# Kernel tuning notes

Hardware: AMD Instinct MI355X
Metric: run time of the kernel (lower is better)

The kernel has to match this reference:

```python
import jax, jax.numpy as jnp
import numpy as np

INITIAL_CAPITAL = 500.0
TRANSACTION_COST = 0.0003
TAU = 1.0  # gumbel-softmax temperature
B, S, F = 256, 4096, 64


def setup_inputs() -> dict:
    key = jax.random.key(0)
    ks = jax.random.split(key, 10)
    features = jax.random.normal(ks[0], (B, S, F), dtype=jnp.float32)
    # make columns 1/2 look like vix level / vix change so branches fire
    features = features.at[:, :, 1].set(20.0 + 10.0 * jax.random.uniform(ks[1], (B, S)))
    features = features.at[:, :, 2].set(0.5 * jax.random.normal(ks[2], (B, S)))
    features = features.at[:, :, 3].set(0.01 * jax.random.normal(ks[3], (B, S)))
    return {
        "features": features,
        "feature_weights": jnp.ones((F,), jnp.float32) / F,
        "long_threshold": jnp.float32(0.52),
        "short_threshold": jnp.float32(0.48),
        "base_position_size": jnp.float32(0.8),
        "conviction_scalar": jnp.float32(0.5),
        "vix_impact": jnp.float32(0.2),
        "vix_collapse_threshold": jnp.float32(0.15),
        "vix_spike_threshold": jnp.float32(0.15),
        "gumbel_noise": jax.random.gumbel(ks[4], (S, B, 3), dtype=jnp.float32),
    }


def reference(features, feature_weights, long_threshold, short_threshold,
              base_position_size, conviction_scalar, vix_impact,
              vix_collapse_threshold, vix_spike_threshold, gumbel_noise):
    batch, seq_len, _ = features.shape
    # predictions: sigmoid of feature-weighted sum  [B,S]
    predictions = jax.nn.sigmoid(jnp.einsum('bsf,f->bs', features, feature_weights))
    # time-major per-step inputs [S,B]
    pred_t = predictions.T
    mom_t = features[:, :, 0].T
    vix_t = features[:, :, 1].T
    vch_t = features[:, :, 2].T
    mret_t = features[:, :, 3].T

    def step(carry, x):
        eq, pos = carry  # eq [B], pos [B,3]
        p, v, dv, m, r, g = x
        signal_strength = jnp.abs(p - 0.5) / 0.5
        vix_collapse = (dv < -vix_collapse_threshold) & (v < 30.0)
        vix_spike = (dv > vix_spike_threshold) & (v > 20.0)
        psz = jnp.clip(base_position_size + conviction_scalar * signal_strength, 0.2, 1.0)
        psz = jnp.where(vix_collapse | vix_spike, psz * (1.0 + vix_impact), psz)
        long_pos = ((p >= long_threshold) & (m > 0)) | vix_collapse
        short_pos = ((p <= short_threshold) & (m < 0)) | vix_spike
        logits = jnp.stack([
            jnp.where(long_pos, 1.0, -10.0),
            jnp.where(short_pos, 1.0, -10.0),
            jnp.where(~long_pos & ~short_pos, 1.0, -10.0),
        ], axis=1)  # [B,3]
        probs = jax.nn.softmax((logits + g) / TAU, axis=1)
        strategy_return = psz * (probs[:, 0] - probs[:, 1]) * r
        position_change = jnp.abs(probs - pos).sum(axis=1)
        eq_new = eq * (1.0 + strategy_return - position_change * TRANSACTION_COST)
        return (eq_new, probs), (eq_new, probs, psz)

    eq0 = jnp.full((batch,), INITIAL_CAPITAL, dtype=features.dtype)
    pos0 = jnp.zeros((batch, 3), features.dtype).at[:, 2].set(1.0)
    (_, _), (eq_seq, pos_seq, psz_seq) = jax.lax.scan(
        step, (eq0, pos0), (pred_t, vix_t, vch_t, mom_t, mret_t, gumbel_noise))
    equity = jnp.concatenate([eq0[:, None], eq_seq.T], axis=1)          # [B,S+1]
    positions = jnp.concatenate([pos0[:, None], jnp.swapaxes(pos_seq, 0, 1)], axis=1)  # [B,S+1,3]
    position_sizes = psz_seq[-1]  # last timestep, matching torch loop leak
    return equity, positions, predictions, position_sizes
```

## Files before the change

### kernel.cpp

```cpp
#include <hip/hip_runtime.h>

#define Bn 256
#define Sn 4096
#define Fn 64
#define TCOST 0.0003f
#define INIT_CAP 500.0f

#define EQ_OFF   0
#define POS_OFF  (Bn * (Sn + 1))
#define PRED_OFF (Bn * (Sn + 1) * 4)
#define PSZ_OFF  (PRED_OFF + Bn * Sn)

#define ROWS_PB 64

__global__ __launch_bounds__(256) void trishot_fwd(
    const float* __restrict__ feat,
    const float* __restrict__ w,
    const float* __restrict__ p_lt, const float* __restrict__ p_st,
    const float* __restrict__ p_bps, const float* __restrict__ p_cs,
    const float* __restrict__ p_vi, const float* __restrict__ p_vct,
    const float* __restrict__ p_vst,
    const float* __restrict__ gumbel,
    float* __restrict__ out)
{
    const int tid  = threadIdx.x;
    const int lane = tid & 63;
    const int wave = tid >> 6;
    const int sub  = lane & 15;
    const int grp  = lane >> 4;

    const float LT = *p_lt, ST = *p_st, BPS = *p_bps, CS = *p_cs,
                VI = *p_vi, VCT = *p_vct, VST = *p_vst;

    const float4 wv = ((const float4*)w)[sub];

    const size_t r0 = (size_t)blockIdx.x * ROWS_PB;

#pragma unroll
    for (int pass = 0; pass < ROWS_PB / 16; ++pass) {
        const size_t row = r0 + (size_t)pass * 16 + (size_t)(wave * 4 + grp);
        const float4 fv = ((const float4*)feat)[row * 16 + sub];

        float x = fv.x * wv.x + fv.y * wv.y + fv.z * wv.z + fv.w * wv.w;
        x += __shfl_xor(x, 1);
        x += __shfl_xor(x, 2);
        x += __shfl_xor(x, 4);
        x += __shfl_xor(x, 8);

        if (sub == 0) {
            const int b = (int)(row >> 12);
            const int s = (int)(row & (Sn - 1));

            const float p = 1.0f / (1.0f + __expf(-x));
            const float mom = fv.x, vix = fv.y, dvix = fv.z, mret = fv.w;

            const float ss = fabsf(p - 0.5f) * 2.0f;
            const bool collapse = (dvix < -VCT) && (vix < 30.0f);
            const bool spike    = (dvix >  VST) && (vix > 20.0f);
            float psz = fminf(fmaxf(BPS + CS * ss, 0.2f), 1.0f);
            if (collapse || spike) psz *= (1.0f + VI);

            const bool lp = ((p >= LT) && (mom > 0.0f)) || collapse;
            const bool sp = ((p <= ST) && (mom < 0.0f)) || spike;
            const float l0 = lp ? 1.0f : -10.0f;
            const float l1 = sp ? 1.0f : -10.0f;
            const float l2 = (!lp && !sp) ? 1.0f : -10.0f;

            const float* g = gumbel + ((size_t)s * Bn + b) * 3;
            const float z0 = l0 + g[0], z1 = l1 + g[1], z2 = l2 + g[2];
            const float zm = fmaxf(z0, fmaxf(z1, z2));
            const float e0 = __expf(z0 - zm), e1 = __expf(z1 - zm),
                        e2 = __expf(z2 - zm);
            const float inv = 1.0f / (e0 + e1 + e2);
            const float q0 = e0 * inv, q1 = e1 * inv, q2 = e2 * inv;

            out[PRED_OFF + row] = p;

            const size_t prow = ((size_t)b * (Sn + 1) + s + 1) * 3;
            float* pos = out + POS_OFF;
            pos[prow + 0] = q0;
            pos[prow + 1] = q1;
            pos[prow + 2] = q2;

            out[EQ_OFF + (size_t)b * (Sn + 1) + s + 1] = psz * (q0 - q1) * mret;

            if (s == 0) {
                const size_t p0row = (size_t)b * (Sn + 1) * 3;
                pos[p0row + 0] = 0.0f;
                pos[p0row + 1] = 0.0f;
                pos[p0row + 2] = 1.0f;
            }
            if (s == Sn - 1) {
                out[PSZ_OFF + b] = psz;
            }
        }
    }
}

#define TB   1024
#define CHB  (Sn / TB)
#define PADi(i) ((i) + ((i) >> 3))

__global__ __launch_bounds__(TB) void trishot_scan(float* __restrict__ out)
{
    const int b = blockIdx.x;
    const int j = threadIdx.x;
    const int lane = j & 63;
    const int wid  = j >> 6;

    float* eq = out + EQ_OFF + (size_t)b * (Sn + 1);
    const float* pos = out + POS_OFF + (size_t)b * (Sn + 1) * 3;

    __shared__ float sfac[Sn + (Sn >> 3)];
    __shared__ float swave[16];

    for (int i = j; i < Sn; i += TB) {
        const float a0 = pos[i * 3 + 0];
        const float a1 = pos[i * 3 + 1];
        const float a2 = pos[i * 3 + 2];
        const float c0 = pos[i * 3 + 3];
        const float c1 = pos[i * 3 + 4];
        const float c2 = pos[i * 3 + 5];
        const float pc = fabsf(c0 - a0) + fabsf(c1 - a1) + fabsf(c2 - a2);
        const float rp = eq[i + 1];
        sfac[PADi(i)] = 1.0f + rp - pc * TCOST;
    }
    __syncthreads();

    const int t0 = j * CHB;
    const float f0 = sfac[PADi(t0 + 0)];
    const float f1 = sfac[PADi(t0 + 1)];
    const float f2 = sfac[PADi(t0 + 2)];
    const float f3 = sfac[PADi(t0 + 3)];
    const float lprod = f0 * f1 * f2 * f3;

    float incl = lprod;
#pragma unroll
    for (int off = 1; off < 64; off <<= 1) {
        const float v = __shfl_up(incl, off);
        if (lane >= off) incl *= v;
    }
    if (lane == 63) swave[wid] = incl;
    __syncthreads();

    if (wid == 0) {
        float wv = (lane < 16) ? swave[lane] : 1.0f;
#pragma unroll
        for (int off = 1; off < 16; off <<= 1) {
            const float v = __shfl_up(wv, off);
            if (lane >= off) wv *= v;
        }
        if (lane < 16) swave[lane] = wv;
    }
    __syncthreads();

    const float woff = (wid > 0) ? swave[wid - 1] : 1.0f;
    float excl = __shfl_up(incl, 1);
    if (lane == 0) excl = 1.0f;
    float eqv = INIT_CAP * woff * excl;
    eqv *= f0; eq[t0 + 1] = eqv;
    eqv *= f1; eq[t0 + 2] = eqv;
    eqv *= f2; eq[t0 + 3] = eqv;
    eqv *= f3; eq[t0 + 4] = eqv;
    if (j == 0) eq[0] = INIT_CAP;
}

extern "C" void kernel_launch(void* const* d_in, const int* in_sizes, int n_in,
                              void* d_out, int out_size, void* d_ws, size_t ws_size,
                              hipStream_t stream) {
    const float* feat   = (const float*)d_in[0];
    const float* w      = (const float*)d_in[1];
    const float* lt     = (const float*)d_in[2];
    const float* st     = (const float*)d_in[3];
    const float* bps    = (const float*)d_in[4];
    const float* cs     = (const float*)d_in[5];
    const float* vi     = (const float*)d_in[6];
    const float* vct    = (const float*)d_in[7];
    const float* vst    = (const float*)d_in[8];
    const float* gumbel = (const float*)d_in[9];
    float* out = (float*)d_out;

    trishot_fwd<<<(Bn * Sn) / ROWS_PB, 256, 0, stream>>>(
        feat, w, lt, st, bps, cs, vi, vct, vst, gumbel, out);
    trishot_scan<<<Bn, TB, 0, stream>>>(out);
}
```

Baseline: 388.1 us.

## Compute per-step equity factors in forward kernel to skip scan's positions reread

The forward kernel now keeps each block's softmax probabilities and raw returns in shared memory and writes the full per-step multiplicative factor, including the transaction cost term. It recomputes the previous row's probabilities for the block boundary. The scan kernel then reads the factors directly instead of rereading the positions array (3 floats per step) and building a shared-memory factor buffer. This removes a large global read in the scan and its LDS staging, at the cost of a small redundant computation and an extra barrier per forward block.

Measured after the change: 386.9 us. About the same (-0.3%).

```diff
diff --git a/kernel.cpp b/kernel.cpp
--- a/kernel.cpp
+++ b/kernel.cpp
@@ -29,16 +29,56 @@
     const int sub  = lane & 15;
     const int grp  = lane >> 4;
 
+    __shared__ float sq0[ROWS_PB + 1];
+    __shared__ float sq1[ROWS_PB + 1];
+    __shared__ float sq2[ROWS_PB + 1];
+    __shared__ float srp[ROWS_PB];
+
     const float LT = *p_lt, ST = *p_st, BPS = *p_bps, CS = *p_cs,
                 VI = *p_vi, VCT = *p_vct, VST = *p_vst;
 
     const float4 wv = ((const float4*)w)[sub];
 
     const size_t r0 = (size_t)blockIdx.x * ROWS_PB;
+    const int b  = (int)(r0 >> 12);
+    const int s0 = (int)(r0 & (Sn - 1));
+
+    if (tid < 16) {
+        float q0p = 0.0f, q1p = 0.0f, q2p = 1.0f;
+        if (s0 != 0) {
+            const float4 fvp = ((const float4*)feat)[(r0 - 1) * 16 + sub];
+            float xp = fvp.x * wv.x + fvp.y * wv.y + fvp.z * wv.z
+                     + fvp.w * wv.w;
+            xp += __shfl_xor(xp, 1);
+            xp += __shfl_xor(xp, 2);
+            xp += __shfl_xor(xp, 4);
+            xp += __shfl_xor(xp, 8);
+            if (tid == 0) {
+                const float p = 1.0f / (1.0f + __expf(-xp));
+                const float mom = fvp.x, vix = fvp.y, dvix = fvp.z;
+                const bool collapse = (dvix < -VCT) && (vix < 30.0f);
+                const bool spike    = (dvix >  VST) && (vix > 20.0f);
+                const bool lp = ((p >= LT) && (mom > 0.0f)) || collapse;
+                const bool sp = ((p <= ST) && (mom < 0.0f)) || spike;
+                const float l0 = lp ? 1.0f : -10.0f;
+                const float l1 = sp ? 1.0f : -10.0f;
+                const float l2 = (!lp && !sp) ? 1.0f : -10.0f;
+                const float* g = gumbel + ((size_t)(s0 - 1) * Bn + b) * 3;
+                const float z0 = l0 + g[0], z1 = l1 + g[1], z2 = l2 + g[2];
+                const float zm = fmaxf(z0, fmaxf(z1, z2));
+                const float e0 = __expf(z0 - zm), e1 = __expf(z1 - zm),
+                            e2 = __expf(z2 - zm);
+                const float inv = 1.0f / (e0 + e1 + e2);
+                q0p = e0 * inv; q1p = e1 * inv; q2p = e2 * inv;
+            }
+        }
+        if (tid == 0) { sq0[0] = q0p; sq1[0] = q1p; sq2[0] = q2p; }
+    }
 
 #pragma unroll
     for (int pass = 0; pass < ROWS_PB / 16; ++pass) {
-        const size_t row = r0 + (size_t)pass * 16 + (size_t)(wave * 4 + grp);
+        const int ridx = pass * 16 + wave * 4 + grp;
+        const size_t row = r0 + (size_t)ridx;
         const float4 fv = ((const float4*)feat)[row * 16 + sub];
 
         float x = fv.x * wv.x + fv.y * wv.y + fv.z * wv.z + fv.w * wv.w;
@@ -48,8 +88,7 @@
         x += __shfl_xor(x, 8);
 
         if (sub == 0) {
-            const int b = (int)(row >> 12);
-            const int s = (int)(row & (Sn - 1));
+            const int s = s0 + ridx;
 
             const float p = 1.0f / (1.0f + __expf(-x));
             const float mom = fv.x, vix = fv.y, dvix = fv.z, mret = fv.w;
@@ -82,24 +121,29 @@
             pos[prow + 1] = q1;
             pos[prow + 2] = q2;
 
-            out[EQ_OFF + (size_t)b * (Sn + 1) + s + 1] = psz * (q0 - q1) * mret;
-
-            if (s == 0) {
-                const size_t p0row = (size_t)b * (Sn + 1) * 3;
-                pos[p0row + 0] = 0.0f;
-                pos[p0row + 1] = 0.0f;
-                pos[p0row + 2] = 1.0f;
-            }
+            sq0[ridx + 1] = q0;
+            sq1[ridx + 1] = q1;
+            sq2[ridx + 1] = q2;
+            srp[ridx]     = psz * (q0 - q1) * mret;
+
             if (s == Sn - 1) {
                 out[PSZ_OFF + b] = psz;
             }
         }
     }
+    __syncthreads();
+
+    if (tid < ROWS_PB) {
+        const float a0 = sq0[tid],     a1 = sq1[tid],     a2 = sq2[tid];
+        const float c0 = sq0[tid + 1], c1 = sq1[tid + 1], c2 = sq2[tid + 1];
+        const float pc = fabsf(c0 - a0) + fabsf(c1 - a1) + fabsf(c2 - a2);
+        out[EQ_OFF + (size_t)b * (Sn + 1) + s0 + tid + 1] =
+            1.0f + srp[tid] - pc * TCOST;
+    }
 }
 
 #define TB   1024
 #define CHB  (Sn / TB)
-#define PADi(i) ((i) + ((i) >> 3))
 
 __global__ __launch_bounds__(TB) void trishot_scan(float* __restrict__ out)
 {
@@ -109,29 +153,14 @@
     const int wid  = j >> 6;
 
     float* eq = out + EQ_OFF + (size_t)b * (Sn + 1);
-    const float* pos = out + POS_OFF + (size_t)b * (Sn + 1) * 3;
-
-    __shared__ float sfac[Sn + (Sn >> 3)];
+
     __shared__ float swave[16];
 
-    for (int i = j; i < Sn; i += TB) {
-        const float a0 = pos[i * 3 + 0];
-        const float a1 = pos[i * 3 + 1];
-        const float a2 = pos[i * 3 + 2];
-        const float c0 = pos[i * 3 + 3];
-        const float c1 = pos[i * 3 + 4];
-        const float c2 = pos[i * 3 + 5];
-        const float pc = fabsf(c0 - a0) + fabsf(c1 - a1) + fabsf(c2 - a2);
-        const float rp = eq[i + 1];
-        sfac[PADi(i)] = 1.0f + rp - pc * TCOST;
-    }
-    __syncthreads();
-
     const int t0 = j * CHB;
-    const float f0 = sfac[PADi(t0 + 0)];
-    const float f1 = sfac[PADi(t0 + 1)];
-    const float f2 = sfac[PADi(t0 + 2)];
-    const float f3 = sfac[PADi(t0 + 3)];
+    const float f0 = eq[t0 + 1];
+    const float f1 = eq[t0 + 2];
+    const float f2 = eq[t0 + 3];
+    const float f3 = eq[t0 + 4];
     const float lprod = f0 * f1 * f2 * f3;
 
     float incl = lprod;
@@ -162,7 +191,14 @@
     eqv *= f1; eq[t0 + 2] = eqv;
     eqv *= f2; eq[t0 + 3] = eqv;
     eqv *= f3; eq[t0 + 4] = eqv;
-    if (j == 0) eq[0] = INIT_CAP;
+
+    if (j == 0) {
+        eq[0] = INIT_CAP;
+        float* pos0 = out + POS_OFF + (size_t)b * (Sn + 1) * 3;
+        pos0[0] = 0.0f;
+        pos0[1] = 0.0f;
+        pos0[2] = 1.0f;
+    }
 }
 
 extern "C" void kernel_launch(void* const* d_in, const int* in_sizes, int n_in,
```
